# Performance work log

Measured on AMD Instinct MI355X. Metric: run time of the kernel, lower is better.

## Reference

```python
import jax, jax.numpy as jnp
import numpy as np

LOW_THRESH = 0.3
HIGH_THRESH = 0.7
BATCH_SIZE = 256
NUM_POS = BATCH_SIZE // 2   # 128; guaranteed <= total_pos since B2=512 GT boxes are scattered positive
NUM_NEG = BATCH_SIZE - NUM_POS


def _xcycwh_to_x1y1x2y2(b):
    xc, yc, w, h = b[..., 0], b[..., 1], b[..., 2], b[..., 3]
    return jnp.stack([xc - w / 2, yc - h / 2, xc + w / 2, yc + h / 2], axis=-1)


def box_iou(box1, box2):
    # box1: (1, B1, 4), box2: (1, B2, 4) in (xc, yc, w, h) -> iou (1, B1, B2)
    area1 = box1[..., 2] * box1[..., 3]              # (1, B1)
    area2 = box2[..., 2] * box2[..., 3]              # (1, B2)
    c1 = _xcycwh_to_x1y1x2y2(box1)[:, :, None, :]    # (1, B1, 1, 4)
    c2 = _xcycwh_to_x1y1x2y2(box2)[:, None, :, :]    # (1, 1, B2, 4)
    x0 = jnp.maximum(c1[..., 0], c2[..., 0])
    y0 = jnp.maximum(c1[..., 1], c2[..., 1])
    x1 = jnp.minimum(c1[..., 2], c2[..., 2])
    y1 = jnp.minimum(c1[..., 3], c2[..., 3])
    inter = jnp.maximum(x1 - x0, 0.0) * jnp.maximum(y1 - y0, 0.0)  # (1, B1, B2)
    return inter / (area1[:, :, None] + area2[:, None, :] - inter)


def setup_inputs() -> dict:
    key = jax.random.key(0)
    k1, k2, k3, k4 = jax.random.split(key, 4)
    return {
        "input_boxes": jax.random.uniform(k1, (1, 50000, 4), dtype=jnp.float32),
        "target_boxes": jax.random.uniform(k2, (1, 512, 4), dtype=jnp.float32),
        "pos_noise": jax.random.uniform(k3, (50000,), dtype=jnp.float32),
        "neg_noise": jax.random.uniform(k4, (50000,), dtype=jnp.float32),
    }


def reference(input_boxes, target_boxes, pos_noise, neg_noise):
    ious = box_iou(input_boxes, target_boxes)        # (1, B1, B2)
    input_max_iou = jnp.max(ious, axis=2)            # (1, B1) best GT per proposal
    input_idx = jnp.argmax(ious, axis=2)             # (1, B1)
    target_idx = jnp.argmax(ious, axis=1)            # (1, B2) best proposal per GT

    pos_mask = input_max_iou[0] > HIGH_THRESH        # (B1,)
    neg_mask = input_max_iou[0] < LOW_THRESH
    # each GT's best-matching proposal is forced positive (scatter_)
    pos_mask = pos_mask.at[target_idx[0]].set(True)
    neg_mask = neg_mask.at[target_idx[0]].set(False)
    # fallback: if no negatives at all, negatives = complement of positives
    neg_mask = jnp.where(jnp.sum(neg_mask) == 0, ~pos_mask, neg_mask)

    # uniform sampling without replacement == top-k over iid uniform noise restricted to the mask
    pos_scores = jnp.where(pos_mask, pos_noise, -1.0)
    _, pos_input_idx = jax.lax.top_k(pos_scores, NUM_POS)      # (NUM_POS,)
    neg_scores = jnp.where(neg_mask, neg_noise, -1.0)
    _, neg_input_idx = jax.lax.top_k(neg_scores, NUM_NEG)      # (NUM_NEG,)

    pos_target_idx = input_idx[0][pos_input_idx]               # (NUM_POS,)
    return pos_input_idx, pos_target_idx, neg_input_idx
```

## Files before the change

kernel.cpp:

```cpp
#include <hip/hip_runtime.h>
#include <stdint.h>

#pragma clang fp contract(off)

typedef unsigned long long ull;

#define HIGHT 0.7f
#define LOWT  0.3f
#define KSEL  128
#define CAP   2048
#define MAXGT 512
#define TPB   256
#define CHUNK 32
#define TJ    128
#define SMP   132
#define NLAD  7
#define NRB   96

__device__ __constant__ float LADV[NLAD] = {0.998f, 0.99f, 0.95f, 0.8f, 0.5f, 0.25f, 0.0625f};

__device__ __forceinline__ float iou_pair(float ax0, float ay0, float ax1, float ay1, float aarea,
                                          float bx0, float by0, float bx1, float by1, float barea){
#pragma clang fp contract(off)
  float x0 = fmaxf(ax0, bx0);
  float y0 = fmaxf(ay0, by0);
  float x1 = fminf(ax1, bx1);
  float y1 = fminf(ay1, by1);
  float dx = fmaxf(x1 - x0, 0.0f);
  float dy = fmaxf(y1 - y0, 0.0f);
  float inter = dx * dy;
  float uni = (aarea + barea) - inter;
  return inter / uni;
}

__global__ __launch_bounds__(TPB)
void fused_iou(const float4* __restrict__ boxes, const float4* __restrict__ gts,
               int n1, int n2, int nblk,
               float* __restrict__ max_iou, int* __restrict__ input_idx,
               ull* __restrict__ colpart, int* __restrict__ forced,
               int* __restrict__ cnts_part, int* __restrict__ cnts,
               ull* __restrict__ colmax,
               const float* __restrict__ pn, const float* __restrict__ nn)
{
#pragma clang fp contract(off)
  const int b = blockIdx.x, t = threadIdx.x;

  for (int x = b * TPB + t; x < n1; x += nblk * TPB) forced[x] = 0;
  if (b == 0){
    if (t < 32) cnts[t] = 0;
    for (int x = t; x < n2; x += TPB) colmax[x] = 0;
  }

  __shared__ float4 gc[MAXGT];
  __shared__ float  ga[MAXGT];
  __shared__ float  smat[CHUNK * SMP];
  __shared__ float  sm[CHUNK];

  for (int j = t; j < n2; j += TPB){
    float4 g = gts[j];
    float hw = g.z * 0.5f, hh = g.w * 0.5f;
    gc[j] = make_float4(g.x - hw, g.y - hh, g.x + hw, g.y + hh);
    ga[j] = g.z * g.w;
  }
  __syncthreads();

  const int lo = b * CHUNK;
  int cr = n1 - lo; if (cr > CHUNK) cr = CHUNK; if (cr < 0) cr = 0;

  const int pi = t >> 3, q = t & 7;
  const bool valid = (pi < cr);
  float px0 = 0, py0 = 0, px1 = 0, py1 = 0, pa = 0;
  if (valid){
    float4 pb = boxes[lo + pi];
    float hw = pb.z * 0.5f, hh = pb.w * 0.5f;
    px0 = pb.x - hw; py0 = pb.y - hh; px1 = pb.x + hw; py1 = pb.y + hh;
    pa = pb.z * pb.w;
  }
  float vA = -1.0f, vB = -1.0f, vC = -1.0f, vD = -1.0f;
  int jA = 0, jB = 0, jC = 0, jD = 0;

  for (int tb = 0; tb < n2; tb += TJ){
    const int tn = min(TJ, n2 - tb);
    if (valid){
      const int jlim = tb + tn;
      int j0 = tb + q;
      for (; j0 + 24 < jlim; j0 += 32){
        const int ja = j0, jb = j0 + 8, jc = j0 + 16, jd = j0 + 24;
        float4 gA = gc[ja]; float aA = ga[ja];
        float4 gB = gc[jb]; float aB = ga[jb];
        float4 gC = gc[jc]; float aC = ga[jc];
        float4 gD = gc[jd]; float aD = ga[jd];
        float u = iou_pair(px0, py0, px1, py1, pa, gA.x, gA.y, gA.z, gA.w, aA);
        float v = iou_pair(px0, py0, px1, py1, pa, gB.x, gB.y, gB.z, gB.w, aB);
        float w = iou_pair(px0, py0, px1, py1, pa, gC.x, gC.y, gC.z, gC.w, aC);
        float x = iou_pair(px0, py0, px1, py1, pa, gD.x, gD.y, gD.z, gD.w, aD);
        smat[pi * SMP + (ja - tb)] = u;
        smat[pi * SMP + (jb - tb)] = v;
        smat[pi * SMP + (jc - tb)] = w;
        smat[pi * SMP + (jd - tb)] = x;
        if (u > vA){ vA = u; jA = ja; }
        if (v > vB){ vB = v; jB = jb; }
        if (w > vC){ vC = w; jC = jc; }
        if (x > vD){ vD = x; jD = jd; }
      }
      for (; j0 < jlim; j0 += 8){
        float4 g0 = gc[j0]; float a0 = ga[j0];
        float u = iou_pair(px0, py0, px1, py1, pa, g0.x, g0.y, g0.z, g0.w, a0);
        smat[pi * SMP + (j0 - tb)] = u;
        if (u > vA){ vA = u; jA = j0; }
      }
    }
    __syncthreads();
    {
      const int jloc = t >> 1, half = t & 1;
      if (jloc < tn){
        float cv = -1.0f; int cp = 0;
        const int p0 = half * 16;
        const int p1 = min(p0 + 16, cr);
        for (int p = p0; p < p1; ++p){
          float v = smat[p * SMP + jloc];
          if (v > cv){ cv = v; cp = p; }
        }
        float ov = __shfl_xor(cv, 1, 64);
        int   op = __shfl_xor(cp, 1, 64);
        if (ov > cv || (ov == cv && op < cp)){ cv = ov; cp = op; }
        if (half == 0){
          colpart[(size_t)b * n2 + (tb + jloc)] =
            ((ull)__float_as_uint(cv) << 32) | (ull)(unsigned)~(unsigned)(lo + cp);
        }
      }
    }
    __syncthreads();
  }

  if (vB > vA || (vB == vA && jB < jA)){ vA = vB; jA = jB; }
  if (vC > vA || (vC == vA && jC < jA)){ vA = vC; jA = jC; }
  if (vD > vA || (vD == vA && jD < jA)){ vA = vD; jA = jD; }
  #pragma unroll
  for (int m = 1; m <= 4; m <<= 1){
    float ov = __shfl_xor(vA, m, 64);
    int   oj = __shfl_xor(jA, m, 64);
    if (ov > vA || (ov == vA && oj < jA)){ vA = ov; jA = oj; }
  }
  if (valid && q == 0){
    max_iou[lo + pi] = vA;
    input_idx[lo + pi] = jA;
    sm[pi] = vA;
  }
  __syncthreads();

  if (t < 64){
    const bool vld = (t < cr);
    float m = vld ? sm[t] : -1.0f;
    bool pos = vld && (m > HIGHT);
    bool nm  = vld && (m < LOWT);
    bool np  = vld && !(m > HIGHT);
    float sp = pos ? pn[lo + t] : -1.0f;
    float sn = (nm || np) ? nn[lo + t] : -1.0f;
    int c[24];
    c[0] = __popcll(__ballot(pos));
    c[1] = __popcll(__ballot(nm));
    c[2] = __popcll(__ballot(np));
    #pragma unroll
    for (int k = 0; k < NLAD; ++k){
      float L = LADV[k];
      c[3 + k]  = __popcll(__ballot(pos && sp > L));
      c[10 + k] = __popcll(__ballot(nm  && sn > L));
      c[17 + k] = __popcll(__ballot(np  && sn > L));
    }
    if (t == 0){
      #pragma unroll
      for (int k = 0; k < 24; ++k) cnts_part[b * 24 + k] = c[k];
    }
  }
}

__global__ __launch_bounds__(TPB)
void colreduce2(const ull* __restrict__ colpart, int n2, int nblk,
                const int* __restrict__ cnts_part,
                int* __restrict__ cnts, ull* __restrict__ colmax)
{
  const int t = threadIdx.x, b = blockIdx.x;
  ull m0 = 0, m1 = 0;
  const int c0 = t, c1 = t + TPB;
  for (int x = b; x < nblk; x += NRB){
    const ull* row = colpart + (size_t)x * n2;
    ull v0 = row[c0];
    ull v1 = (c1 < n2) ? row[c1] : 0;
    if (v0 > m0) m0 = v0;
    if (v1 > m1) m1 = v1;
  }
  if (c0 < n2 && m0) atomicMax(&colmax[c0], m0);
  if (c1 < n2 && m1) atomicMax(&colmax[c1], m1);

  if (t < 24){
    int s = 0;
    for (int x = b; x < nblk; x += NRB) s += cnts_part[x * 24 + t];
    if (s) atomicAdd(&cnts[t], s);
  }
}

__global__ __launch_bounds__(512)
void forcefix(const ull* __restrict__ colmax, int n1, int n2,
              const float* __restrict__ max_iou,
              const float* __restrict__ pn, const float* __restrict__ nn,
              int* __restrict__ forced, int* __restrict__ cnts)
{
  const int t = threadIdx.x;
  if (t >= n2) return;
  ull key = colmax[t];
  unsigned idx = ~(unsigned)(key & 0xFFFFFFFFull);
  if (idx >= (unsigned)n1) return;
  int old = atomicExch(&forced[idx], 1);
  if (old != 0) return;
  float m2 = max_iou[idx];
  if (m2 > HIGHT) return;
  float sp = pn[idx];
  float sn = nn[idx];
  atomicAdd(&cnts[0], 1);
  atomicAdd(&cnts[2], -1);
  #pragma unroll
  for (int k = 0; k < NLAD; ++k){
    float L = LADV[k];
    if (sp > L) atomicAdd(&cnts[3 + k], 1);
    if (sn > L) atomicAdd(&cnts[17 + k], -1);
  }
  if (m2 < LOWT){
    atomicAdd(&cnts[1], -1);
    #pragma unroll
    for (int k = 0; k < NLAD; ++k)
      if (sn > LADV[k]) atomicAdd(&cnts[10 + k], -1);
  }
}

__device__ __forceinline__ float pick_tau(const int* lad, int tot){
  if (tot <= CAP) return -1.0f;
  for (int k = 0; k < NLAD; ++k)
    if (lad[k] >= KSEL) return LADV[k];
  return -1.0f;
}

__global__ __launch_bounds__(TPB)
void collect_kernel(const float* __restrict__ max_iou, const int* __restrict__ forced,
                    const float* __restrict__ pn, const float* __restrict__ nn,
                    int n1, int* __restrict__ cnts, ull* __restrict__ cand)
{
  __shared__ int s_c[24];
  const int t = threadIdx.x;
  if (t < 24) s_c[t] = cnts[t];
  __syncthreads();
  const bool fb = (s_c[1] == 0);
  const int totP = s_c[0];
  const int totN = fb ? s_c[2] : s_c[1];
  const float tauP = pick_tau(&s_c[3], totP);
  const float tauN = pick_tau(fb ? &s_c[17] : &s_c[10], totN);

  const int i = blockIdx.x * TPB + t;
  if (i >= n1) return;
  float m = max_iou[i];
  bool f = forced[i] != 0;
  bool pos = (m > HIGHT) || f;
  if (pos){
    float sc = pn[i];
    if (sc > tauP){
      int p = atomicAdd(&cnts[24], 1);
      if (p < CAP) cand[p] = ((ull)(__float_as_uint(sc) + 1u) << 32) | (ull)(unsigned)~(unsigned)i;
    }
  } else if (totP < KSEL && i < 2 * KSEL){
    int p = atomicAdd(&cnts[24], 1);
    if (p < CAP) cand[p] = (ull)(unsigned)~(unsigned)i;
  }
  bool seln = fb ? (!pos) : ((m < LOWT) && !f);
  if (seln){
    float sc = nn[i];
    if (sc > tauN){
      int p = atomicAdd(&cnts[25], 1);
      if (p < CAP) cand[CAP + p] = ((ull)(__float_as_uint(sc) + 1u) << 32) | (ull)(unsigned)~(unsigned)i;
    }
  } else if (totN < KSEL && i < 2 * KSEL){
    int p = atomicAdd(&cnts[25], 1);
    if (p < CAP) cand[CAP + p] = (ull)(unsigned)~(unsigned)i;
  }
}

__global__ __launch_bounds__(1024)
void select_kernel(const ull* __restrict__ cand, const int* __restrict__ cnts,
                   const int* __restrict__ input_idx, int* __restrict__ out)
{
  const int t = threadIdx.x;
  const bool isPos = (blockIdx.x == 0);
  __shared__ ull keys[CAP];
  int n = cnts[isPos ? 24 : 25]; if (n > CAP) n = CAP;
  for (int x = t; x < n; x += 1024)
    keys[x] = cand[(isPos ? 0 : CAP) + x];
  __syncthreads();
  ull mk[2]; int mr[2];
  #pragma unroll
  for (int e = 0; e < 2; ++e){
    int x = t + e * 1024;
    mk[e] = (x < n) ? keys[x] : ~0ull;
    mr[e] = 0;
  }
  for (int o = 0; o < n; ++o){
    ull ko = keys[o];
    #pragma unroll
    for (int e = 0; e < 2; ++e) mr[e] += (ko > mk[e]);
  }
  #pragma unroll
  for (int e = 0; e < 2; ++e){
    int x = t + e * 1024;
    if (x < n && mr[e] < KSEL){
      unsigned idx = ~(unsigned)(mk[e] & 0xFFFFFFFFull);
      if (isPos){ out[mr[e]] = (int)idx; out[KSEL + mr[e]] = input_idx[idx]; }
      else        out[2 * KSEL + mr[e]] = (int)idx;
    }
  }
}

extern "C" void kernel_launch(void* const* d_in, const int* in_sizes, int n_in,
                              void* d_out, int out_size, void* d_ws, size_t ws_size,
                              hipStream_t stream){
  const float4* boxes = (const float4*)d_in[0];
  const float4* gts   = (const float4*)d_in[1];
  const float* pos_noise = (const float*)d_in[2];
  const float* neg_noise = (const float*)d_in[3];
  const int n1 = in_sizes[0] / 4;
  const int n2 = in_sizes[1] / 4;
  int* out = (int*)d_out;

  char* ws = (char*)d_ws;
  size_t off = 0;
  auto carve = [&](size_t bytes) -> char* {
    char* p = ws + off;
    off = (off + bytes + 255) & ~(size_t)255;
    return p;
  };
  const int nblk = (n1 + CHUNK - 1) / CHUNK;
  float* max_iou   = (float*)carve((size_t)n1 * 4);
  int*   input_idx = (int*)  carve((size_t)n1 * 4);
  ull*   colpart   = (ull*)  carve((size_t)nblk * n2 * 8);
  int*   forced    = (int*)  carve((size_t)n1 * 4);
  int*   cnts_part = (int*)  carve((size_t)nblk * 24 * 4);
  int*   cnts      = (int*)  carve(32 * 4);
  ull*   colmax    = (ull*)  carve((size_t)MAXGT * 8);
  ull*   cand      = (ull*)  carve((size_t)2 * CAP * 8);

  const int gb = (n1 + TPB - 1) / TPB;
  fused_iou<<<nblk, TPB, 0, stream>>>(boxes, gts, n1, n2, nblk,
                                      max_iou, input_idx, colpart, forced,
                                      cnts_part, cnts, colmax, pos_noise, neg_noise);
  colreduce2<<<NRB, TPB, 0, stream>>>(colpart, n2, nblk, cnts_part, cnts, colmax);
  forcefix<<<1, 512, 0, stream>>>(colmax, n1, n2, max_iou,
                                  pos_noise, neg_noise, forced, cnts);
  collect_kernel<<<gb, TPB, 0, stream>>>(max_iou, forced, pos_noise, neg_noise,
                                         n1, cnts, cand);
  select_kernel<<<2, 1024, 0, stream>>>(cand, cnts, input_idx, out);
}
```

Before: 130.7 us.

## Fuse column reduction with force fix and collection with selection

Merges the column-max reduction and the forced-positive fixup into one kernel that reduces columns in shared memory per block, removing the global colmax buffer and its atomics. Merges candidate collection and top-k selection into a single two-block kernel that scans all proposals and gathers candidates in shared memory. This cuts two launches and the global candidate round-trip. In exchange, collection now runs on only two blocks, which serialises the full scan onto two CUs.

```diff
diff --git a/kernel.cpp b/kernel.cpp
--- a/kernel.cpp
+++ b/kernel.cpp
@@ -15,7 +15,6 @@
 #define TJ    128
 #define SMP   132
 #define NLAD  7
-#define NRB   96
 
 __device__ __constant__ float LADV[NLAD] = {0.998f, 0.99f, 0.95f, 0.8f, 0.5f, 0.25f, 0.0625f};
 
@@ -39,17 +38,13 @@
                float* __restrict__ max_iou, int* __restrict__ input_idx,
                ull* __restrict__ colpart, int* __restrict__ forced,
                int* __restrict__ cnts_part, int* __restrict__ cnts,
-               ull* __restrict__ colmax,
                const float* __restrict__ pn, const float* __restrict__ nn)
 {
 #pragma clang fp contract(off)
   const int b = blockIdx.x, t = threadIdx.x;
 
   for (int x = b * TPB + t; x < n1; x += nblk * TPB) forced[x] = 0;
-  if (b == 0){
-    if (t < 32) cnts[t] = 0;
-    for (int x = t; x < n2; x += TPB) colmax[x] = 0;
-  }
+  if (b == 0 && t < 32) cnts[t] = 0;
 
   __shared__ float4 gc[MAXGT];
   __shared__ float  ga[MAXGT];
@@ -175,125 +170,136 @@
   }
 }
 
-__global__ __launch_bounds__(TPB)
-void colreduce2(const ull* __restrict__ colpart, int n2, int nblk,
-                const int* __restrict__ cnts_part,
-                int* __restrict__ cnts, ull* __restrict__ colmax)
+__global__ __launch_bounds__(512)
+void colfix3(const ull* __restrict__ colpart, int n1, int n2, int nblk,
+             const float* __restrict__ max_iou,
+             const float* __restrict__ pn, const float* __restrict__ nn,
+             int* __restrict__ forced, const int* __restrict__ cnts_part,
+             int* __restrict__ cnts)
 {
-  const int t = threadIdx.x, b = blockIdx.x;
-  ull m0 = 0, m1 = 0;
-  const int c0 = t, c1 = t + TPB;
-  for (int x = b; x < nblk; x += NRB){
-    const ull* row = colpart + (size_t)x * n2;
-    ull v0 = row[c0];
-    ull v1 = (c1 < n2) ? row[c1] : 0;
-    if (v0 > m0) m0 = v0;
-    if (v1 > m1) m1 = v1;
-  }
-  if (c0 < n2 && m0) atomicMax(&colmax[c0], m0);
-  if (c1 < n2 && m1) atomicMax(&colmax[c1], m1);
-
+  const int t = threadIdx.x, b = blockIdx.x, nb = gridDim.x;
+  const int c = b * 8 + (t & 7);
+  const int s = t >> 3;
+  ull m = 0;
+  if (c < n2){
+    for (int r = s; r < nblk; r += 64){
+      ull v = colpart[(size_t)r * n2 + c];
+      if (v > m) m = v;
+    }
+  }
+  __shared__ ull cm[8][64];
+  cm[t & 7][s] = m;
+
+  int csum = 0;
   if (t < 24){
-    int s = 0;
-    for (int x = b; x < nblk; x += NRB) s += cnts_part[x * 24 + t];
-    if (s) atomicAdd(&cnts[t], s);
-  }
-}
-
-__global__ __launch_bounds__(512)
-void forcefix(const ull* __restrict__ colmax, int n1, int n2,
-              const float* __restrict__ max_iou,
-              const float* __restrict__ pn, const float* __restrict__ nn,
-              int* __restrict__ forced, int* __restrict__ cnts)
-{
-  const int t = threadIdx.x;
-  if (t >= n2) return;
-  ull key = colmax[t];
-  unsigned idx = ~(unsigned)(key & 0xFFFFFFFFull);
-  if (idx >= (unsigned)n1) return;
-  int old = atomicExch(&forced[idx], 1);
-  if (old != 0) return;
-  float m2 = max_iou[idx];
-  if (m2 > HIGHT) return;
-  float sp = pn[idx];
-  float sn = nn[idx];
-  atomicAdd(&cnts[0], 1);
-  atomicAdd(&cnts[2], -1);
-  #pragma unroll
-  for (int k = 0; k < NLAD; ++k){
-    float L = LADV[k];
-    if (sp > L) atomicAdd(&cnts[3 + k], 1);
-    if (sn > L) atomicAdd(&cnts[17 + k], -1);
-  }
-  if (m2 < LOWT){
-    atomicAdd(&cnts[1], -1);
-    #pragma unroll
-    for (int k = 0; k < NLAD; ++k)
-      if (sn > LADV[k]) atomicAdd(&cnts[10 + k], -1);
-  }
-}
-
-__device__ __forceinline__ float pick_tau(const int* lad, int tot){
-  if (tot <= CAP) return -1.0f;
+    for (int x = b; x < nblk; x += nb) csum += cnts_part[x * 24 + t];
+  }
+  __syncthreads();
+  if (t < 24 && csum) atomicAdd(&cnts[t], csum);
+
+  if (t < 8){
+    const int cc = b * 8 + t;
+    if (cc < n2){
+      ull best = 0;
+      for (int k = 0; k < 64; ++k){ ull v = cm[t][k]; if (v > best) best = v; }
+      unsigned idx = ~(unsigned)(best & 0xFFFFFFFFull);
+      if (idx < (unsigned)n1){
+        int old = atomicExch(&forced[idx], 1);
+        if (old == 0){
+          float m2 = max_iou[idx];
+          if (!(m2 > HIGHT)){
+            float sp = pn[idx];
+            float sn = nn[idx];
+            atomicAdd(&cnts[0], 1);
+            atomicAdd(&cnts[2], -1);
+            #pragma unroll
+            for (int k = 0; k < NLAD; ++k){
+              float L = LADV[k];
+              if (sp > L) atomicAdd(&cnts[3 + k], 1);
+              if (sn > L) atomicAdd(&cnts[17 + k], -1);
+            }
+            if (m2 < LOWT){
+              atomicAdd(&cnts[1], -1);
+              #pragma unroll
+              for (int k = 0; k < NLAD; ++k)
+                if (sn > LADV[k]) atomicAdd(&cnts[10 + k], -1);
+            }
+          }
+        }
+      }
+    }
+  }
+}
+
+__device__ __forceinline__ float pick_tau2(const int* lad){
   for (int k = 0; k < NLAD; ++k)
     if (lad[k] >= KSEL) return LADV[k];
   return -1.0f;
 }
 
-__global__ __launch_bounds__(TPB)
-void collect_kernel(const float* __restrict__ max_iou, const int* __restrict__ forced,
-                    const float* __restrict__ pn, const float* __restrict__ nn,
-                    int n1, int* __restrict__ cnts, ull* __restrict__ cand)
-{
-  __shared__ int s_c[24];
-  const int t = threadIdx.x;
-  if (t < 24) s_c[t] = cnts[t];
-  __syncthreads();
-  const bool fb = (s_c[1] == 0);
-  const int totP = s_c[0];
-  const int totN = fb ? s_c[2] : s_c[1];
-  const float tauP = pick_tau(&s_c[3], totP);
-  const float tauN = pick_tau(fb ? &s_c[17] : &s_c[10], totN);
-
-  const int i = blockIdx.x * TPB + t;
-  if (i >= n1) return;
-  float m = max_iou[i];
-  bool f = forced[i] != 0;
-  bool pos = (m > HIGHT) || f;
-  if (pos){
-    float sc = pn[i];
-    if (sc > tauP){
-      int p = atomicAdd(&cnts[24], 1);
-      if (p < CAP) cand[p] = ((ull)(__float_as_uint(sc) + 1u) << 32) | (ull)(unsigned)~(unsigned)i;
-    }
-  } else if (totP < KSEL && i < 2 * KSEL){
-    int p = atomicAdd(&cnts[24], 1);
-    if (p < CAP) cand[p] = (ull)(unsigned)~(unsigned)i;
-  }
-  bool seln = fb ? (!pos) : ((m < LOWT) && !f);
-  if (seln){
-    float sc = nn[i];
-    if (sc > tauN){
-      int p = atomicAdd(&cnts[25], 1);
-      if (p < CAP) cand[CAP + p] = ((ull)(__float_as_uint(sc) + 1u) << 32) | (ull)(unsigned)~(unsigned)i;
-    }
-  } else if (totN < KSEL && i < 2 * KSEL){
-    int p = atomicAdd(&cnts[25], 1);
-    if (p < CAP) cand[CAP + p] = (ull)(unsigned)~(unsigned)i;
-  }
-}
-
 __global__ __launch_bounds__(1024)
-void select_kernel(const ull* __restrict__ cand, const int* __restrict__ cnts,
-                   const int* __restrict__ input_idx, int* __restrict__ out)
+void finalize(const float* __restrict__ max_iou, const int* __restrict__ forced,
+              const float* __restrict__ pn, const float* __restrict__ nn,
+              const int* __restrict__ cnts, const int* __restrict__ input_idx,
+              int n1, int* __restrict__ out)
 {
   const int t = threadIdx.x;
   const bool isPos = (blockIdx.x == 0);
+  __shared__ int s_c[24];
+  __shared__ int lcnt;
   __shared__ ull keys[CAP];
-  int n = cnts[isPos ? 24 : 25]; if (n > CAP) n = CAP;
-  for (int x = t; x < n; x += 1024)
-    keys[x] = cand[(isPos ? 0 : CAP) + x];
-  __syncthreads();
+  if (t < 24) s_c[t] = cnts[t];
+  if (t == 0) lcnt = 0;
+  __syncthreads();
+  const bool fb = (s_c[1] == 0);
+  const int totM = isPos ? s_c[0] : (fb ? s_c[2] : s_c[1]);
+  const float tau = isPos ? pick_tau2(&s_c[3]) : pick_tau2(fb ? &s_c[17] : &s_c[10]);
+  const float* noise = isPos ? pn : nn;
+  const bool fillOn = (totM < KSEL);
+
+  const int n4 = n1 >> 2;
+  for (int v = t; v < n4; v += 1024){
+    const float4 m4 = reinterpret_cast<const float4*>(max_iou)[v];
+    const int4  f4 = reinterpret_cast<const int4*>(forced)[v];
+    const float4 s4 = reinterpret_cast<const float4*>(noise)[v];
+    #pragma unroll
+    for (int e = 0; e < 4; ++e){
+      const float m  = (e==0)?m4.x:(e==1)?m4.y:(e==2)?m4.z:m4.w;
+      const int   f  = (e==0)?f4.x:(e==1)?f4.y:(e==2)?f4.z:f4.w;
+      const float sc = (e==0)?s4.x:(e==1)?s4.y:(e==2)?s4.z:s4.w;
+      const int i = v * 4 + e;
+      const bool pos = (m > HIGHT) || (f != 0);
+      const bool sel = isPos ? pos : (fb ? (!pos) : ((m < LOWT) && f == 0));
+      if (sel){
+        if (sc > tau){
+          int p = atomicAdd(&lcnt, 1);
+          if (p < CAP) keys[p] = ((ull)(__float_as_uint(sc) + 1u) << 32) | (ull)(unsigned)~(unsigned)i;
+        }
+      } else if (fillOn && i < 2 * KSEL){
+        int p = atomicAdd(&lcnt, 1);
+        if (p < CAP) keys[p] = (ull)(unsigned)~(unsigned)i;
+      }
+    }
+  }
+  for (int i = (n4 << 2) + t; i < n1; i += 1024){
+    const float m = max_iou[i];
+    const int   f = forced[i];
+    const float sc = noise[i];
+    const bool pos = (m > HIGHT) || (f != 0);
+    const bool sel = isPos ? pos : (fb ? (!pos) : ((m < LOWT) && f == 0));
+    if (sel){
+      if (sc > tau){
+        int p = atomicAdd(&lcnt, 1);
+        if (p < CAP) keys[p] = ((ull)(__float_as_uint(sc) + 1u) << 32) | (ull)(unsigned)~(unsigned)i;
+      }
+    } else if (fillOn && i < 2 * KSEL){
+      int p = atomicAdd(&lcnt, 1);
+      if (p < CAP) keys[p] = (ull)(unsigned)~(unsigned)i;
+    }
+  }
+  __syncthreads();
+
+  int n = lcnt; if (n > CAP) n = CAP;
   ull mk[2]; int mr[2];
   #pragma unroll
   for (int e = 0; e < 2; ++e){
@@ -303,8 +309,8 @@
   }
   for (int o = 0; o < n; ++o){
     ull ko = keys[o];
-    #pragma unroll
-    for (int e = 0; e < 2; ++e) mr[e] += (ko > mk[e]);
+    mr[0] += (ko > mk[0]);
+    mr[1] += (ko > mk[1]);
   }
   #pragma unroll
   for (int e = 0; e < 2; ++e){
@@ -342,17 +348,13 @@
   int*   forced    = (int*)  carve((size_t)n1 * 4);
   int*   cnts_part = (int*)  carve((size_t)nblk * 24 * 4);
   int*   cnts      = (int*)  carve(32 * 4);
-  ull*   colmax    = (ull*)  carve((size_t)MAXGT * 8);
-  ull*   cand      = (ull*)  carve((size_t)2 * CAP * 8);
-
-  const int gb = (n1 + TPB - 1) / TPB;
+
   fused_iou<<<nblk, TPB, 0, stream>>>(boxes, gts, n1, n2, nblk,
                                       max_iou, input_idx, colpart, forced,
-                                      cnts_part, cnts, colmax, pos_noise, neg_noise);
-  colreduce2<<<NRB, TPB, 0, stream>>>(colpart, n2, nblk, cnts_part, cnts, colmax);
-  forcefix<<<1, 512, 0, stream>>>(colmax, n1, n2, max_iou,
-                                  pos_noise, neg_noise, forced, cnts);
-  collect_kernel<<<gb, TPB, 0, stream>>>(max_iou, forced, pos_noise, neg_noise,
-                                         n1, cnts, cand);
-  select_kernel<<<2, 1024, 0, stream>>>(cand, cnts, input_idx, out);
-}
+                                      cnts_part, cnts, pos_noise, neg_noise);
+  const int cb = (n2 + 7) / 8;
+  colfix3<<<cb, 512, 0, stream>>>(colpart, n1, n2, nblk, max_iou,
+                                  pos_noise, neg_noise, forced, cnts_part, cnts);
+  finalize<<<2, 1024, 0, stream>>>(max_iou, forced, pos_noise, neg_noise,
+                                   cnts, input_idx, n1, out);
+}
```

Measured after the change: 139.6 us. 6.8% more time.

## Register-block two proposals per thread and fuse column reduce with forced-positive fix

Applied to the files above, without the earlier changes.

Each thread now computes IoUs for two proposals against the same ground-truth boxes, so every shared-memory GT load is reused twice. The per-block chunk grows to 64 proposals, which halves the number of blocks and the size of the column-partial buffer. The column-max reduction and the forced-positive fixup are merged into one kernel, with the last-arriving block doing the fixup, which removes a launch. The candidate threshold is now taken from the ladder even when the total count is small. The risks are higher register and shared-memory pressure, and the last-block pattern depends on the counter at cnts[26] being reset on every call.

```diff
diff --git a/kernel.cpp b/kernel.cpp
--- a/kernel.cpp
+++ b/kernel.cpp
@@ -11,7 +11,7 @@
 #define CAP   2048
 #define MAXGT 512
 #define TPB   256
-#define CHUNK 32
+#define CHUNK 64
 #define TJ    128
 #define SMP   132
 #define NLAD  7
@@ -68,20 +68,30 @@
   int cr = n1 - lo; if (cr > CHUNK) cr = CHUNK; if (cr < 0) cr = 0;
 
   const int pi = t >> 3, q = t & 7;
-  const bool valid = (pi < cr);
-  float px0 = 0, py0 = 0, px1 = 0, py1 = 0, pa = 0;
-  if (valid){
+  const bool validA = (pi < cr);
+  const bool validB = (pi + 32 < cr);
+  float ax0 = 0, ay0 = 0, ax1 = 0, ay1 = 0, aa = 0;
+  float bx0 = 0, by0 = 0, bx1 = 0, by1 = 0, ba = 0;
+  if (validA){
     float4 pb = boxes[lo + pi];
     float hw = pb.z * 0.5f, hh = pb.w * 0.5f;
-    px0 = pb.x - hw; py0 = pb.y - hh; px1 = pb.x + hw; py1 = pb.y + hh;
-    pa = pb.z * pb.w;
+    ax0 = pb.x - hw; ay0 = pb.y - hh; ax1 = pb.x + hw; ay1 = pb.y + hh;
+    aa = pb.z * pb.w;
+  }
+  if (validB){
+    float4 pb = boxes[lo + pi + 32];
+    float hw = pb.z * 0.5f, hh = pb.w * 0.5f;
+    bx0 = pb.x - hw; by0 = pb.y - hh; bx1 = pb.x + hw; by1 = pb.y + hh;
+    ba = pb.z * pb.w;
   }
   float vA = -1.0f, vB = -1.0f, vC = -1.0f, vD = -1.0f;
   int jA = 0, jB = 0, jC = 0, jD = 0;
+  float wA = -1.0f, wB = -1.0f, wC = -1.0f, wD = -1.0f;
+  int kA = 0, kB = 0, kC = 0, kD = 0;
 
   for (int tb = 0; tb < n2; tb += TJ){
     const int tn = min(TJ, n2 - tb);
-    if (valid){
+    {
       const int jlim = tb + tn;
       int j0 = tb + q;
       for (; j0 + 24 < jlim; j0 += 32){
@@ -90,24 +100,47 @@
         float4 gB = gc[jb]; float aB = ga[jb];
         float4 gC = gc[jc]; float aC = ga[jc];
         float4 gD = gc[jd]; float aD = ga[jd];
-        float u = iou_pair(px0, py0, px1, py1, pa, gA.x, gA.y, gA.z, gA.w, aA);
-        float v = iou_pair(px0, py0, px1, py1, pa, gB.x, gB.y, gB.z, gB.w, aB);
-        float w = iou_pair(px0, py0, px1, py1, pa, gC.x, gC.y, gC.z, gC.w, aC);
-        float x = iou_pair(px0, py0, px1, py1, pa, gD.x, gD.y, gD.z, gD.w, aD);
-        smat[pi * SMP + (ja - tb)] = u;
-        smat[pi * SMP + (jb - tb)] = v;
-        smat[pi * SMP + (jc - tb)] = w;
-        smat[pi * SMP + (jd - tb)] = x;
-        if (u > vA){ vA = u; jA = ja; }
-        if (v > vB){ vB = v; jB = jb; }
-        if (w > vC){ vC = w; jC = jc; }
-        if (x > vD){ vD = x; jD = jd; }
+        if (validA){
+          float u = iou_pair(ax0, ay0, ax1, ay1, aa, gA.x, gA.y, gA.z, gA.w, aA);
+          float v = iou_pair(ax0, ay0, ax1, ay1, aa, gB.x, gB.y, gB.z, gB.w, aB);
+          float w = iou_pair(ax0, ay0, ax1, ay1, aa, gC.x, gC.y, gC.z, gC.w, aC);
+          float x = iou_pair(ax0, ay0, ax1, ay1, aa, gD.x, gD.y, gD.z, gD.w, aD);
+          smat[pi * SMP + (ja - tb)] = u;
+          smat[pi * SMP + (jb - tb)] = v;
+          smat[pi * SMP + (jc - tb)] = w;
+          smat[pi * SMP + (jd - tb)] = x;
+          if (u > vA){ vA = u; jA = ja; }
+          if (v > vB){ vB = v; jB = jb; }
+          if (w > vC){ vC = w; jC = jc; }
+          if (x > vD){ vD = x; jD = jd; }
+        }
+        if (validB){
+          float u = iou_pair(bx0, by0, bx1, by1, ba, gA.x, gA.y, gA.z, gA.w, aA);
+          float v = iou_pair(bx0, by0, bx1, by1, ba, gB.x, gB.y, gB.z, gB.w, aB);
+          float w = iou_pair(bx0, by0, bx1, by1, ba, gC.x, gC.y, gC.z, gC.w, aC);
+          float x = iou_pair(bx0, by0, bx1, by1, ba, gD.x, gD.y, gD.z, gD.w, aD);
+          smat[(pi + 32) * SMP + (ja - tb)] = u;
+          smat[(pi + 32) * SMP + (jb - tb)] = v;
+          smat[(pi + 32) * SMP + (jc - tb)] = w;
+          smat[(pi + 32) * SMP + (jd - tb)] = x;
+          if (u > wA){ wA = u; kA = ja; }
+          if (v > wB){ wB = v; kB = jb; }
+          if (w > wC){ wC = w; kC = jc; }
+          if (x > wD){ wD = x; kD = jd; }
+        }
       }
       for (; j0 < jlim; j0 += 8){
         float4 g0 = gc[j0]; float a0 = ga[j0];
-        float u = iou_pair(px0, py0, px1, py1, pa, g0.x, g0.y, g0.z, g0.w, a0);
-        smat[pi * SMP + (j0 - tb)] = u;
-        if (u > vA){ vA = u; jA = j0; }
+        if (validA){
+          float u = iou_pair(ax0, ay0, ax1, ay1, aa, g0.x, g0.y, g0.z, g0.w, a0);
+          smat[pi * SMP + (j0 - tb)] = u;
+          if (u > vA){ vA = u; jA = j0; }
+        }
+        if (validB){
+          float u = iou_pair(bx0, by0, bx1, by1, ba, g0.x, g0.y, g0.z, g0.w, a0);
+          smat[(pi + 32) * SMP + (j0 - tb)] = u;
+          if (u > wA){ wA = u; kA = j0; }
+        }
       }
     }
     __syncthreads();
@@ -115,8 +148,8 @@
       const int jloc = t >> 1, half = t & 1;
       if (jloc < tn){
         float cv = -1.0f; int cp = 0;
-        const int p0 = half * 16;
-        const int p1 = min(p0 + 16, cr);
+        const int p0 = half * 32;
+        const int p1 = min(p0 + 32, cr);
         for (int p = p0; p < p1; ++p){
           float v = smat[p * SMP + jloc];
           if (v > cv){ cv = v; cp = p; }
@@ -136,16 +169,27 @@
   if (vB > vA || (vB == vA && jB < jA)){ vA = vB; jA = jB; }
   if (vC > vA || (vC == vA && jC < jA)){ vA = vC; jA = jC; }
   if (vD > vA || (vD == vA && jD < jA)){ vA = vD; jA = jD; }
+  if (wB > wA || (wB == wA && kB < kA)){ wA = wB; kA = kB; }
+  if (wC > wA || (wC == wA && kC < kA)){ wA = wC; kA = kC; }
+  if (wD > wA || (wD == wA && kD < kA)){ wA = wD; kA = kD; }
   #pragma unroll
   for (int m = 1; m <= 4; m <<= 1){
     float ov = __shfl_xor(vA, m, 64);
     int   oj = __shfl_xor(jA, m, 64);
     if (ov > vA || (ov == vA && oj < jA)){ vA = ov; jA = oj; }
-  }
-  if (valid && q == 0){
+    float ow = __shfl_xor(wA, m, 64);
+    int   ok = __shfl_xor(kA, m, 64);
+    if (ow > wA || (ow == wA && ok < kA)){ wA = ow; kA = ok; }
+  }
+  if (validA && q == 0){
     max_iou[lo + pi] = vA;
     input_idx[lo + pi] = jA;
     sm[pi] = vA;
+  }
+  if (validB && q == 0){
+    max_iou[lo + pi + 32] = wA;
+    input_idx[lo + pi + 32] = kA;
+    sm[pi + 32] = wA;
   }
   __syncthreads();
 
@@ -176,9 +220,11 @@
 }
 
 __global__ __launch_bounds__(TPB)
-void colreduce2(const ull* __restrict__ colpart, int n2, int nblk,
-                const int* __restrict__ cnts_part,
-                int* __restrict__ cnts, ull* __restrict__ colmax)
+void colfix(const ull* __restrict__ colpart, int n1, int n2, int nblk,
+            const float* __restrict__ max_iou,
+            const float* __restrict__ pn, const float* __restrict__ nn,
+            int* __restrict__ forced, const int* __restrict__ cnts_part,
+            int* __restrict__ cnts, ull* __restrict__ colmax)
 {
   const int t = threadIdx.x, b = blockIdx.x;
   ull m0 = 0, m1 = 0;
@@ -198,43 +244,45 @@
     for (int x = b; x < nblk; x += NRB) s += cnts_part[x * 24 + t];
     if (s) atomicAdd(&cnts[t], s);
   }
-}
-
-__global__ __launch_bounds__(512)
-void forcefix(const ull* __restrict__ colmax, int n1, int n2,
-              const float* __restrict__ max_iou,
-              const float* __restrict__ pn, const float* __restrict__ nn,
-              int* __restrict__ forced, int* __restrict__ cnts)
-{
-  const int t = threadIdx.x;
-  if (t >= n2) return;
-  ull key = colmax[t];
-  unsigned idx = ~(unsigned)(key & 0xFFFFFFFFull);
-  if (idx >= (unsigned)n1) return;
-  int old = atomicExch(&forced[idx], 1);
-  if (old != 0) return;
-  float m2 = max_iou[idx];
-  if (m2 > HIGHT) return;
-  float sp = pn[idx];
-  float sn = nn[idx];
-  atomicAdd(&cnts[0], 1);
-  atomicAdd(&cnts[2], -1);
-  #pragma unroll
-  for (int k = 0; k < NLAD; ++k){
-    float L = LADV[k];
-    if (sp > L) atomicAdd(&cnts[3 + k], 1);
-    if (sn > L) atomicAdd(&cnts[17 + k], -1);
-  }
-  if (m2 < LOWT){
-    atomicAdd(&cnts[1], -1);
-    #pragma unroll
-    for (int k = 0; k < NLAD; ++k)
-      if (sn > LADV[k]) atomicAdd(&cnts[10 + k], -1);
-  }
-}
-
-__device__ __forceinline__ float pick_tau(const int* lad, int tot){
-  if (tot <= CAP) return -1.0f;
+
+  __threadfence();
+  __syncthreads();
+  __shared__ int islast;
+  if (t == 0) islast = (atomicAdd(&cnts[26], 1) == NRB - 1) ? 1 : 0;
+  __syncthreads();
+  if (!islast) return;
+
+  for (int j = t; j < n2; j += TPB){
+    ull key = __hip_atomic_load(&colmax[j], __ATOMIC_RELAXED, __HIP_MEMORY_SCOPE_AGENT);
+    unsigned idx = ~(unsigned)(key & 0xFFFFFFFFull);
+    if (idx < (unsigned)n1){
+      int old = atomicExch(&forced[idx], 1);
+      if (old == 0){
+        float m2 = max_iou[idx];
+        if (!(m2 > HIGHT)){
+          float sp = pn[idx];
+          float sn = nn[idx];
+          atomicAdd(&cnts[0], 1);
+          atomicAdd(&cnts[2], -1);
+          #pragma unroll
+          for (int k = 0; k < NLAD; ++k){
+            float L = LADV[k];
+            if (sp > L) atomicAdd(&cnts[3 + k], 1);
+            if (sn > L) atomicAdd(&cnts[17 + k], -1);
+          }
+          if (m2 < LOWT){
+            atomicAdd(&cnts[1], -1);
+            #pragma unroll
+            for (int k = 0; k < NLAD; ++k)
+              if (sn > LADV[k]) atomicAdd(&cnts[10 + k], -1);
+          }
+        }
+      }
+    }
+  }
+}
+
+__device__ __forceinline__ float pick_tau2(const int* lad){
   for (int k = 0; k < NLAD; ++k)
     if (lad[k] >= KSEL) return LADV[k];
   return -1.0f;
@@ -252,8 +300,8 @@
   const bool fb = (s_c[1] == 0);
   const int totP = s_c[0];
   const int totN = fb ? s_c[2] : s_c[1];
-  const float tauP = pick_tau(&s_c[3], totP);
-  const float tauN = pick_tau(fb ? &s_c[17] : &s_c[10], totN);
+  const float tauP = pick_tau2(&s_c[3]);
+  const float tauN = pick_tau2(fb ? &s_c[17] : &s_c[10]);
 
   const int i = blockIdx.x * TPB + t;
   if (i >= n1) return;
@@ -349,9 +397,8 @@
   fused_iou<<<nblk, TPB, 0, stream>>>(boxes, gts, n1, n2, nblk,
                                       max_iou, input_idx, colpart, forced,
                                       cnts_part, cnts, colmax, pos_noise, neg_noise);
-  colreduce2<<<NRB, TPB, 0, stream>>>(colpart, n2, nblk, cnts_part, cnts, colmax);
-  forcefix<<<1, 512, 0, stream>>>(colmax, n1, n2, max_iou,
-                                  pos_noise, neg_noise, forced, cnts);
+  colfix<<<NRB, TPB, 0, stream>>>(colpart, n1, n2, nblk, max_iou,
+                                  pos_noise, neg_noise, forced, cnts_part, cnts, colmax);
   collect_kernel<<<gb, TPB, 0, stream>>>(max_iou, forced, pos_noise, neg_noise,
                                          n1, cnts, cand);
   select_kernel<<<2, 1024, 0, stream>>>(cand, cnts, input_idx, out);
```

Result: slower. 137.4 us (+5.1%).

## Fuse five kernels into three using last-block-done atomics

Applied to the files above, without the earlier changes.

Merges the column reduce and force-fix kernels into one, with the last finishing block doing the fix-up. It also merges candidate collection and top-k selection, with the last block running the rank-based selection for both positive and negative sets in 256 threads. This removes two kernel launches and their gaps. In exchange, the selection runs serially on a single 256-thread block with 8 slots per thread rather than two 1024-thread blocks. The change also drops the tot<=CAP shortcut in the tau choice and relies on counters cnts[26] and cnts[27] being zeroed beforehand.

```diff
diff --git a/kernel.cpp b/kernel.cpp
--- a/kernel.cpp
+++ b/kernel.cpp
@@ -16,6 +16,7 @@
 #define SMP   132
 #define NLAD  7
 #define NRB   96
+#define SLOTS (CAP / TPB)
 
 __device__ __constant__ float LADV[NLAD] = {0.998f, 0.99f, 0.95f, 0.8f, 0.5f, 0.25f, 0.0625f};
 
@@ -176,9 +177,11 @@
 }
 
 __global__ __launch_bounds__(TPB)
-void colreduce2(const ull* __restrict__ colpart, int n2, int nblk,
-                const int* __restrict__ cnts_part,
-                int* __restrict__ cnts, ull* __restrict__ colmax)
+void colfix(const ull* __restrict__ colpart, int n1, int n2, int nblk,
+            const float* __restrict__ max_iou,
+            const float* __restrict__ pn, const float* __restrict__ nn,
+            int* __restrict__ forced, const int* __restrict__ cnts_part,
+            int* __restrict__ cnts, ull* __restrict__ colmax)
 {
   const int t = threadIdx.x, b = blockIdx.x;
   ull m0 = 0, m1 = 0;
@@ -198,52 +201,55 @@
     for (int x = b; x < nblk; x += NRB) s += cnts_part[x * 24 + t];
     if (s) atomicAdd(&cnts[t], s);
   }
-}
-
-__global__ __launch_bounds__(512)
-void forcefix(const ull* __restrict__ colmax, int n1, int n2,
-              const float* __restrict__ max_iou,
-              const float* __restrict__ pn, const float* __restrict__ nn,
-              int* __restrict__ forced, int* __restrict__ cnts)
-{
-  const int t = threadIdx.x;
-  if (t >= n2) return;
-  ull key = colmax[t];
-  unsigned idx = ~(unsigned)(key & 0xFFFFFFFFull);
-  if (idx >= (unsigned)n1) return;
-  int old = atomicExch(&forced[idx], 1);
-  if (old != 0) return;
-  float m2 = max_iou[idx];
-  if (m2 > HIGHT) return;
-  float sp = pn[idx];
-  float sn = nn[idx];
-  atomicAdd(&cnts[0], 1);
-  atomicAdd(&cnts[2], -1);
-  #pragma unroll
-  for (int k = 0; k < NLAD; ++k){
-    float L = LADV[k];
-    if (sp > L) atomicAdd(&cnts[3 + k], 1);
-    if (sn > L) atomicAdd(&cnts[17 + k], -1);
-  }
-  if (m2 < LOWT){
-    atomicAdd(&cnts[1], -1);
-    #pragma unroll
-    for (int k = 0; k < NLAD; ++k)
-      if (sn > LADV[k]) atomicAdd(&cnts[10 + k], -1);
-  }
-}
-
-__device__ __forceinline__ float pick_tau(const int* lad, int tot){
-  if (tot <= CAP) return -1.0f;
+
+  __threadfence();
+  __syncthreads();
+  __shared__ int islast;
+  if (t == 0) islast = (atomicAdd(&cnts[26], 1) == NRB - 1) ? 1 : 0;
+  __syncthreads();
+  if (!islast) return;
+
+  for (int j = t; j < n2; j += TPB){
+    ull key = __hip_atomic_load(&colmax[j], __ATOMIC_RELAXED, __HIP_MEMORY_SCOPE_AGENT);
+    unsigned idx = ~(unsigned)(key & 0xFFFFFFFFull);
+    if (idx < (unsigned)n1){
+      int old = atomicExch(&forced[idx], 1);
+      if (old == 0){
+        float m2 = max_iou[idx];
+        if (!(m2 > HIGHT)){
+          float sp = pn[idx];
+          float sn = nn[idx];
+          atomicAdd(&cnts[0], 1);
+          atomicAdd(&cnts[2], -1);
+          #pragma unroll
+          for (int k = 0; k < NLAD; ++k){
+            float L = LADV[k];
+            if (sp > L) atomicAdd(&cnts[3 + k], 1);
+            if (sn > L) atomicAdd(&cnts[17 + k], -1);
+          }
+          if (m2 < LOWT){
+            atomicAdd(&cnts[1], -1);
+            #pragma unroll
+            for (int k = 0; k < NLAD; ++k)
+              if (sn > LADV[k]) atomicAdd(&cnts[10 + k], -1);
+          }
+        }
+      }
+    }
+  }
+}
+
+__device__ __forceinline__ float pick_tau2(const int* lad){
   for (int k = 0; k < NLAD; ++k)
     if (lad[k] >= KSEL) return LADV[k];
   return -1.0f;
 }
 
 __global__ __launch_bounds__(TPB)
-void collect_kernel(const float* __restrict__ max_iou, const int* __restrict__ forced,
+void collect_select(const float* __restrict__ max_iou, const int* __restrict__ forced,
                     const float* __restrict__ pn, const float* __restrict__ nn,
-                    int n1, int* __restrict__ cnts, ull* __restrict__ cand)
+                    int n1, int* __restrict__ cnts, ull* __restrict__ cand,
+                    const int* __restrict__ input_idx, int* __restrict__ out)
 {
   __shared__ int s_c[24];
   const int t = threadIdx.x;
@@ -252,68 +258,75 @@
   const bool fb = (s_c[1] == 0);
   const int totP = s_c[0];
   const int totN = fb ? s_c[2] : s_c[1];
-  const float tauP = pick_tau(&s_c[3], totP);
-  const float tauN = pick_tau(fb ? &s_c[17] : &s_c[10], totN);
+  const float tauP = pick_tau2(&s_c[3]);
+  const float tauN = pick_tau2(fb ? &s_c[17] : &s_c[10]);
 
   const int i = blockIdx.x * TPB + t;
-  if (i >= n1) return;
-  float m = max_iou[i];
-  bool f = forced[i] != 0;
-  bool pos = (m > HIGHT) || f;
-  if (pos){
-    float sc = pn[i];
-    if (sc > tauP){
+  if (i < n1){
+    float m = max_iou[i];
+    bool f = forced[i] != 0;
+    bool pos = (m > HIGHT) || f;
+    if (pos){
+      float sc = pn[i];
+      if (sc > tauP){
+        int p = atomicAdd(&cnts[24], 1);
+        if (p < CAP) cand[p] = ((ull)(__float_as_uint(sc) + 1u) << 32) | (ull)(unsigned)~(unsigned)i;
+      }
+    } else if (totP < KSEL && i < 2 * KSEL){
       int p = atomicAdd(&cnts[24], 1);
-      if (p < CAP) cand[p] = ((ull)(__float_as_uint(sc) + 1u) << 32) | (ull)(unsigned)~(unsigned)i;
-    }
-  } else if (totP < KSEL && i < 2 * KSEL){
-    int p = atomicAdd(&cnts[24], 1);
-    if (p < CAP) cand[p] = (ull)(unsigned)~(unsigned)i;
-  }
-  bool seln = fb ? (!pos) : ((m < LOWT) && !f);
-  if (seln){
-    float sc = nn[i];
-    if (sc > tauN){
+      if (p < CAP) cand[p] = (ull)(unsigned)~(unsigned)i;
+    }
+    bool seln = fb ? (!pos) : ((m < LOWT) && !f);
+    if (seln){
+      float sc = nn[i];
+      if (sc > tauN){
+        int p = atomicAdd(&cnts[25], 1);
+        if (p < CAP) cand[CAP + p] = ((ull)(__float_as_uint(sc) + 1u) << 32) | (ull)(unsigned)~(unsigned)i;
+      }
+    } else if (totN < KSEL && i < 2 * KSEL){
       int p = atomicAdd(&cnts[25], 1);
-      if (p < CAP) cand[CAP + p] = ((ull)(__float_as_uint(sc) + 1u) << 32) | (ull)(unsigned)~(unsigned)i;
-    }
-  } else if (totN < KSEL && i < 2 * KSEL){
-    int p = atomicAdd(&cnts[25], 1);
-    if (p < CAP) cand[CAP + p] = (ull)(unsigned)~(unsigned)i;
-  }
-}
-
-__global__ __launch_bounds__(1024)
-void select_kernel(const ull* __restrict__ cand, const int* __restrict__ cnts,
-                   const int* __restrict__ input_idx, int* __restrict__ out)
-{
-  const int t = threadIdx.x;
-  const bool isPos = (blockIdx.x == 0);
+      if (p < CAP) cand[CAP + p] = (ull)(unsigned)~(unsigned)i;
+    }
+  }
+
+  __threadfence();
+  __syncthreads();
+  __shared__ int islast;
+  if (t == 0) islast = (atomicAdd(&cnts[27], 1) == (int)gridDim.x - 1) ? 1 : 0;
+  __syncthreads();
+  if (!islast) return;
+  __threadfence();
+
   __shared__ ull keys[CAP];
-  int n = cnts[isPos ? 24 : 25]; if (n > CAP) n = CAP;
-  for (int x = t; x < n; x += 1024)
-    keys[x] = cand[(isPos ? 0 : CAP) + x];
-  __syncthreads();
-  ull mk[2]; int mr[2];
-  #pragma unroll
-  for (int e = 0; e < 2; ++e){
-    int x = t + e * 1024;
-    mk[e] = (x < n) ? keys[x] : ~0ull;
-    mr[e] = 0;
-  }
-  for (int o = 0; o < n; ++o){
-    ull ko = keys[o];
+  for (int mode = 0; mode < 2; ++mode){
+    const bool isPos = (mode == 0);
+    int n = __hip_atomic_load(&cnts[isPos ? 24 : 25], __ATOMIC_RELAXED, __HIP_MEMORY_SCOPE_AGENT);
+    if (n > CAP) n = CAP;
+    for (int x = t; x < n; x += TPB)
+      keys[x] = __hip_atomic_load(&cand[(isPos ? 0 : CAP) + x], __ATOMIC_RELAXED, __HIP_MEMORY_SCOPE_AGENT);
+    __syncthreads();
+    ull mk[SLOTS]; int mr[SLOTS];
     #pragma unroll
-    for (int e = 0; e < 2; ++e) mr[e] += (ko > mk[e]);
-  }
-  #pragma unroll
-  for (int e = 0; e < 2; ++e){
-    int x = t + e * 1024;
-    if (x < n && mr[e] < KSEL){
-      unsigned idx = ~(unsigned)(mk[e] & 0xFFFFFFFFull);
-      if (isPos){ out[mr[e]] = (int)idx; out[KSEL + mr[e]] = input_idx[idx]; }
-      else        out[2 * KSEL + mr[e]] = (int)idx;
-    }
+    for (int e = 0; e < SLOTS; ++e){
+      int x = t + e * TPB;
+      mk[e] = (x < n) ? keys[x] : ~0ull;
+      mr[e] = 0;
+    }
+    for (int o = 0; o < n; ++o){
+      ull ko = keys[o];
+      #pragma unroll
+      for (int e = 0; e < SLOTS; ++e) mr[e] += (ko > mk[e]);
+    }
+    #pragma unroll
+    for (int e = 0; e < SLOTS; ++e){
+      int x = t + e * TPB;
+      if (x < n && mr[e] < KSEL){
+        unsigned idx = ~(unsigned)(mk[e] & 0xFFFFFFFFull);
+        if (isPos){ out[mr[e]] = (int)idx; out[KSEL + mr[e]] = input_idx[idx]; }
+        else        out[2 * KSEL + mr[e]] = (int)idx;
+      }
+    }
+    __syncthreads();
   }
 }
 
@@ -349,10 +362,8 @@
   fused_iou<<<nblk, TPB, 0, stream>>>(boxes, gts, n1, n2, nblk,
                                       max_iou, input_idx, colpart, forced,
                                       cnts_part, cnts, colmax, pos_noise, neg_noise);
-  colreduce2<<<NRB, TPB, 0, stream>>>(colpart, n2, nblk, cnts_part, cnts, colmax);
-  forcefix<<<1, 512, 0, stream>>>(colmax, n1, n2, max_iou,
-                                  pos_noise, neg_noise, forced, cnts);
-  collect_kernel<<<gb, TPB, 0, stream>>>(max_iou, forced, pos_noise, neg_noise,
-                                         n1, cnts, cand);
-  select_kernel<<<2, 1024, 0, stream>>>(cand, cnts, input_idx, out);
-}
+  colfix<<<NRB, TPB, 0, stream>>>(colpart, n1, n2, nblk, max_iou,
+                                  pos_noise, neg_noise, forced, cnts_part, cnts, colmax);
+  collect_select<<<gb, TPB, 0, stream>>>(max_iou, forced, pos_noise, neg_noise,
+                                         n1, cnts, cand, input_idx, out);
+}
```

Measured after the change: 155.9 us. 1.19x slower.
